# Kernel tuning notes

Hardware: AMD Instinct MI355X
Metric: run time of the kernel (lower is better)

Reference implementation:

```python
import jax, jax.numpy as jnp
import numpy as np

Q, C, T = 256, 128, 128
L = Q + C + T            # 512
D = 1024                 # d_model
H = 8                    # heads
DK = D // H              # 128 = self_attn.d_k
F = 3                    # num_latent_relations
R = 50                   # num_relation_kinds = len(relations2id)
FF = 4 * D               # feed-forward hidden
DEFAULT_QQ_ID = 0        # relations2id['q:q-default']
EPS = 1e-5


def setup_inputs():
    key = jax.random.key(0)
    ks = jax.random.split(key, 40)
    s = 0.02
    def nrm(k, shape, scale=s):
        return jax.random.normal(k, shape, jnp.float32) * scale
    inp = {
        'x': jax.random.normal(ks[0], (1, L, D), jnp.float32),
        'qc_relation': jax.random.uniform(ks[1], (Q, C, F), jnp.float32),
        'cq_relation': jax.random.uniform(ks[2], (C, Q, F), jnp.float32),
        'qt_relation': jax.random.uniform(ks[3], (Q, T, F), jnp.float32),
        'tq_relation': jax.random.uniform(ks[4], (T, Q, F), jnp.float32),
        'ct_relation': jax.random.randint(ks[5], (C + T, C + T), 0, R, jnp.int32),
        'predefined_relation': jax.random.randint(ks[6], (L, L), 0, R, jnp.int32),
        'mask': jnp.ones((1, L, L), jnp.int32),
        # relation embedding tables
        'rel_k_emb': nrm(ks[7], (R, DK)), 'rel_v_emb': nrm(ks[8], (R, DK)),
        'lqc_k': nrm(ks[9], (F, DK)), 'lqc_v': nrm(ks[10], (F, DK)),
        'lcq_k': nrm(ks[11], (F, DK)), 'lcq_v': nrm(ks[12], (F, DK)),
        'lqt_k': nrm(ks[13], (F, DK)), 'lqt_v': nrm(ks[14], (F, DK)),
        'ltq_k': nrm(ks[15], (F, DK)), 'ltq_v': nrm(ks[16], (F, DK)),
        # attention projections (torch Linear: y = x @ W.T + b)
        'Wq': nrm(ks[17], (D, D)), 'bq': jnp.zeros((D,), jnp.float32),
        'Wk': nrm(ks[18], (D, D)), 'bk': jnp.zeros((D,), jnp.float32),
        'Wv': nrm(ks[19], (D, D)), 'bv': jnp.zeros((D,), jnp.float32),
        'Wo': nrm(ks[20], (D, D)), 'bo': jnp.zeros((D,), jnp.float32),
        # layer norms
        'ln1_g': jnp.ones((D,), jnp.float32), 'ln1_b': jnp.zeros((D,), jnp.float32),
        'ln2_g': jnp.ones((D,), jnp.float32), 'ln2_b': jnp.zeros((D,), jnp.float32),
        # FFN
        'W1': nrm(ks[21], (FF, D)), 'b1': jnp.zeros((FF,), jnp.float32),
        'W2': nrm(ks[22], (D, FF)), 'b2': jnp.zeros((D,), jnp.float32),
    }
    return inp


def layer_norm(x, g, b):
    m = jnp.mean(x, -1, keepdims=True)
    v = jnp.mean((x - m) ** 2, -1, keepdims=True)
    return (x - m) * jax.lax.rsqrt(v + EPS) * g + b


def build_latent_relation(ct, qc, cq, qt, tq, emb, lqc, lcq, lqt, ltq):
    # qq block: every entry is the default-qq embedding row
    qq = jnp.broadcast_to(emb[DEFAULT_QQ_ID], (Q, Q, DK))
    qc_e = jnp.einsum('qcf,fd->qcd', qc, lqc)
    cq_e = jnp.einsum('cqf,fd->cqd', cq, lcq)
    qt_e = jnp.einsum('qtf,fd->qtd', qt, lqt)
    tq_e = jnp.einsum('tqf,fd->tqd', tq, ltq)
    ct_e = emb[ct]                                      # [(c+t),(c+t),DK]
    top = jnp.concatenate([qq, qc_e, qt_e], axis=1)      # [Q, L, DK]
    bot = jnp.concatenate([jnp.concatenate([cq_e, tq_e], 0), ct_e], axis=1)  # [C+T, L, DK]
    return jnp.concatenate([top, bot], axis=0)           # [L, L, DK]


def relation_attention(x, rel_k, rel_v, mask, Wq, bq, Wk, bk, Wv, bv, Wo, bo):
    B = x.shape[0]
    def proj(W, b):
        return (x @ W.T + b).reshape(B, L, H, DK).transpose(0, 2, 1, 3)  # [B,H,L,DK]
    q, k, v = proj(Wq, bq), proj(Wk, bk), proj(Wv, bv)
    scores = (jnp.einsum('bhid,bhjd->bhij', q, k)
              + jnp.einsum('bhid,ijd->bhij', q, rel_k)) / jnp.sqrt(jnp.float32(DK))
    scores = jnp.where(mask[:, None] == 0, jnp.float32(-1e9), scores)
    p = jax.nn.softmax(scores, axis=-1)
    o = (jnp.einsum('bhij,bhjd->bhid', p, v)
         + jnp.einsum('bhij,ijd->bhid', p, rel_v))
    o = o.transpose(0, 2, 1, 3).reshape(B, L, D)
    return o @ Wo.T + bo


def reference(x, qc_relation, cq_relation, qt_relation, tq_relation,
              ct_relation, predefined_relation, mask,
              rel_k_emb, rel_v_emb, lqc_k, lqc_v, lcq_k, lcq_v,
              lqt_k, lqt_v, ltq_k, ltq_v,
              Wq, bq, Wk, bk, Wv, bv, Wo, bo,
              ln1_g, ln1_b, ln2_g, ln2_b, W1, b1, W2, b2):
    # latent relation build + combine with predefined lookup
    rel_k = (rel_k_emb[predefined_relation]
             + build_latent_relation(ct_relation, qc_relation, cq_relation,
                                     qt_relation, tq_relation,
                                     rel_k_emb, lqc_k, lcq_k, lqt_k, ltq_k))
    rel_v = (rel_v_emb[predefined_relation]
             + build_latent_relation(ct_relation, qc_relation, cq_relation,
                                     qt_relation, tq_relation,
                                     rel_v_emb, lqc_v, lcq_v, lqt_v, ltq_v))
    # sublayer 0: pre-norm relation-biased self attention (dropout=0)
    h = x + relation_attention(layer_norm(x, ln1_g, ln1_b), rel_k, rel_v, mask,
                               Wq, bq, Wk, bk, Wv, bv, Wo, bo)
    # sublayer 1: pre-norm FFN
    y = layer_norm(h, ln2_g, ln2_b)
    ffn = jax.nn.relu(y @ W1.T + b1) @ W2.T + b2
    return h + ffn
```

## Files before the change

### kernel.cpp

```cpp
#include <hip/hip_runtime.h>
#include <hip/hip_bf16.h>

#define LL 512
#define DD 1024
#define HH 8
#define DKK 128
#define QQ 256
#define CCC 128
#define TTT 128
#define RR 50
#define FFF 4096

typedef __attribute__((ext_vector_type(8))) short short8;
typedef __attribute__((ext_vector_type(4))) float float4v;

__device__ __forceinline__ unsigned short f2bu(float f) {
  __hip_bfloat16 h = __float2bfloat16(f);
  unsigned short u; __builtin_memcpy(&u, &h, 2); return u;
}
__device__ __forceinline__ float b2f(unsigned short u) {
  unsigned int v = ((unsigned int)u) << 16;
  float f; __builtin_memcpy(&f, &v, 4); return f;
}
__device__ __forceinline__ int4 cvt8(float4 x, float4 y) {
  int4 o;
  o.x = (int)f2bu(x.x) | ((int)f2bu(x.y) << 16);
  o.y = (int)f2bu(x.z) | ((int)f2bu(x.w) << 16);
  o.z = (int)f2bu(y.x) | ((int)f2bu(y.y) << 16);
  o.w = (int)f2bu(y.z) | ((int)f2bu(y.w) << 16);
  return o;
}

__device__ __forceinline__ void lds_barrier() {
  __builtin_amdgcn_sched_barrier(0);
  __builtin_amdgcn_s_waitcnt(0xC07F);
  __builtin_amdgcn_s_barrier();
  __builtin_amdgcn_sched_barrier(0);
}

#define LOADSET(A0,A1,B0,B1,F0,F1,F2,F3,itv) { int k0v = (itv) << 6;          \
  A0 = *(const int4*)(Az + (size_t)(bm + r)*lda + k0v + gc*8);                \
  A1 = *(const int4*)(Az + (size_t)(bm + 32 + r)*lda + k0v + gc*8);           \
  if constexpr (!CONVB) {                                                     \
    B0 = *(const int4*)(Bz16 + (size_t)(bnb + r)*ldb + k0v + gc*8);           \
    if constexpr (NB > 1)                                                     \
      B1 = *(const int4*)(Bz16 + (size_t)(bnb + 32 + r)*ldb + k0v + gc*8);    \
  } else {                                                                    \
    F0 = *(const float4*)(Bz32 + (size_t)(bnb + r)*ldb + k0v + gc*8);         \
    F1 = *(const float4*)(Bz32 + (size_t)(bnb + r)*ldb + k0v + gc*8 + 4);     \
    if constexpr (NB > 1) {                                                   \
      F2 = *(const float4*)(Bz32 + (size_t)(bnb + 32 + r)*ldb + k0v + gc*8);  \
      F3 = *(const float4*)(Bz32 + (size_t)(bnb + 32 + r)*ldb + k0v + gc*8 + 4); } } }

#define STORESET2(basep,A0,A1,B0,B1,F0,F1,F2,F3) {                            \
  char* bse = (basep);                                                        \
  *(int4*)(bse + r*128 + sl*16) = A0;                                         \
  *(int4*)(bse + (32 + r)*128 + sl*16) = A1;                                  \
  if constexpr (!CONVB) {                                                     \
    *(int4*)(bse + ABYTES + r*128 + sl*16) = B0;                              \
    if constexpr (NB > 1)                                                     \
      *(int4*)(bse + ABYTES + (32 + r)*128 + sl*16) = B1;                     \
  } else {                                                                    \
    *(int4*)(bse + ABYTES + r*128 + sl*16) = cvt8(F0, F1);                    \
    if constexpr (NB > 1)                                                     \
      *(int4*)(bse + ABYTES + (32 + r)*128 + sl*16) = cvt8(F2, F3); } }

__global__ __launch_bounds__(256) void ln_bf16_kernel(const float* __restrict__ x,
    const float* __restrict__ g, const float* __restrict__ b,
    unsigned short* __restrict__ y)
{
  int row = blockIdx.x, t = threadIdx.x;
  const float4 xv = ((const float4*)(x + row*DD))[t];
  float s  = xv.x+xv.y+xv.z+xv.w;
  float ss = xv.x*xv.x+xv.y*xv.y+xv.z*xv.z+xv.w*xv.w;
  __shared__ float rs[256], rss[256];
  rs[t]=s; rss[t]=ss; __syncthreads();
  for (int st=128; st>0; st>>=1){ if (t<st){ rs[t]+=rs[t+st]; rss[t]+=rss[t+st]; } __syncthreads(); }
  float mean = rs[0] * (1.0f/DD);
  float var  = rss[0]*(1.0f/DD) - mean*mean;
  float inv  = rsqrtf(var + 1e-5f);
  float4 gv = ((const float4*)g)[t], bv = ((const float4*)b)[t];
  ushort4 ov;
  ov.x = f2bu((xv.x-mean)*inv*gv.x + bv.x);
  ov.y = f2bu((xv.y-mean)*inv*gv.y + bv.y);
  ov.z = f2bu((xv.z-mean)*inv*gv.z + bv.z);
  ov.w = f2bu((xv.w-mean)*inv*gv.w + bv.w);
  ((ushort4*)(y + row*DD))[t] = ov;
}

__global__ __launch_bounds__(256) void addbias_kernel(float* __restrict__ out,
                                                      const float* __restrict__ b2)
{
  int g = blockIdx.x*256 + threadIdx.x;
  out[g] += b2[g & (DD-1)];
}

template<int BN, int CONVB, int ZK, int OUT_BF16, int RELU, int HAS_SRC, int HAS_BIAS>
__global__ __launch_bounds__(256) void gemm_pl(
    const unsigned short* __restrict__ A, int lda, size_t sAz,
    const void* __restrict__ Bv, int ldb, size_t sBz,
    const float* __restrict__ bias,
    const float* __restrict__ src, int ldsrc, size_t sSz,
    void* __restrict__ Cv, int ldc, size_t sCz,
    int K)
{
  constexpr int BM = 64;
  constexpr int WM = 32, WN = BN/2, FM = 2, FN = WN/16;
  constexpr int NB = BN/32;
  constexpr int ABYTES = BM*128, TILE = ABYTES + BN*128;
  __shared__ char lds[2*TILE];
  int t = threadIdx.x, w = t >> 6, l = t & 63;
  size_t z = blockIdx.z;
  const unsigned short* Az = A + z*sAz;
  const unsigned short* Bz16 = (const unsigned short*)Bv + (CONVB ? 0 : z*sBz);
  const float*          Bz32 = (const float*)Bv + (CONVB ? z*sBz : 0);
  int bm = blockIdx.y*BM, bn = blockIdx.x*BN;
  int bnb = bn;
  int wm = (w>>1)*WM, wn = (w&1)*WN;

  float4v acc[FM][FN];
  #pragma unroll
  for (int m=0;m<FM;++m)
    #pragma unroll
    for (int n=0;n<FN;++n) acc[m][n] = (float4v){0.f,0.f,0.f,0.f};

  int r = t >> 3, sl = t & 7;
  int gc = sl ^ (r & 7);
  int quad = l >> 4, lrow = l & 15;
  const int nit = K >> 6;

  int4 pa0, pa1, pb0, pb1;  float4 pf0, pf1, pf2, pf3;
  int4 qa0, qa1, qb0, qb1;  float4 qf0, qf1, qf2, qf3;

  auto compute = [&](const char* base) {
    const char* ab = base;
    const char* bb = base + ABYTES;
    #pragma unroll
    for (int step=0; step<2; ++step) {
      int c = step*4 + quad;
      short8 af[FM], bf[FN];
      #pragma unroll
      for (int m=0;m<FM;++m) {
        int Rw = wm + m*16 + lrow;
        af[m] = *(const short8*)(ab + Rw*128 + ((c ^ (Rw & 7))*16));
      }
      #pragma unroll
      for (int n=0;n<FN;++n) {
        int Rw = wn + n*16 + lrow;
        bf[n] = *(const short8*)(bb + Rw*128 + ((c ^ (Rw & 7))*16));
      }
      #pragma unroll
      for (int m=0;m<FM;++m)
        #pragma unroll
        for (int n=0;n<FN;++n)
          acc[m][n] = __builtin_amdgcn_mfma_f32_16x16x32_bf16(af[m], bf[n], acc[m][n], 0, 0, 0);
    }
  };

  LOADSET(pa0,pa1,pb0,pb1,pf0,pf1,pf2,pf3, 0);
  LOADSET(qa0,qa1,qb0,qb1,qf0,qf1,qf2,qf3, 1);
  for (int it = 0; it < nit; it += 2) {
    STORESET2(lds, pa0,pa1,pb0,pb1,pf0,pf1,pf2,pf3);
    if (it + 2 < nit) LOADSET(pa0,pa1,pb0,pb1,pf0,pf1,pf2,pf3, it+2);
    lds_barrier();
    compute(lds);
    STORESET2(lds + TILE, qa0,qa1,qb0,qb1,qf0,qf1,qf2,qf3);
    if (it + 3 < nit) LOADSET(qa0,qa1,qb0,qb1,qf0,qf1,qf2,qf3, it+3);
    lds_barrier();
    compute(lds + TILE);
  }

  #pragma unroll
  for (int m=0;m<FM;++m)
    #pragma unroll
    for (int n=0;n<FN;++n)
      #pragma unroll
      for (int rg=0;rg<4;++rg) {
        int row = bm + wm + m*16 + quad*4 + rg;
        int col = bn + wn + n*16 + lrow;
        float vv = acc[m][n][rg];
        if (ZK) {
          atomicAdd(&((float*)Cv)[(size_t)row*ldc + col], vv);
        } else {
          if (HAS_BIAS) vv += bias[col];
          if (HAS_SRC)  vv += src[z*sSz + (size_t)row*ldsrc + col];
          if (RELU) vv = fmaxf(vv, 0.f);
          if (OUT_BF16) ((unsigned short*)Cv)[z*sCz + (size_t)row*ldc + col] = f2bu(vv);
          else          ((float*)Cv)[z*sCz + (size_t)row*ldc + col] = vv;
        }
      }
}

__global__ __launch_bounds__(256) void gemm_qkv_pl(
    const unsigned short* __restrict__ A,
    const float* __restrict__ Wq, const float* __restrict__ Wk,
    const float* __restrict__ Wv,
    const float* __restrict__ bq, const float* __restrict__ bk,
    const float* __restrict__ bv,
    unsigned short* __restrict__ Qh, unsigned short* __restrict__ Kh,
    unsigned short* __restrict__ Vt)
{
  constexpr int BN = 64, CONVB = 1;
  constexpr int WM = 32, WN = 32, FM = 2, FN = 2;
  constexpr int NB = 2;
  constexpr int ABYTES = 64*128, TILE = ABYTES + BN*128;
  __shared__ char lds[2*TILE];
  int t = threadIdx.x, w = t >> 6, l = t & 63;
  int bm = blockIdx.y*64, bn = blockIdx.x*BN;
  int wm = (w>>1)*WM, wn = (w&1)*WN;
  const int lda = DD, ldb = DD, nit = DD >> 6;
  const unsigned short* Az = A;
  int part0 = bn >> 10;
  const float* Bz32 = (part0==0 ? Wq : part0==1 ? Wk : Wv) + (size_t)(bn & 1023)*DD;
  const unsigned short* Bz16 = nullptr; (void)Bz16;
  int bnb = 0;

  float4v acc[FM][FN];
  #pragma unroll
  for (int m=0;m<FM;++m)
    #pragma unroll
    for (int n=0;n<FN;++n) acc[m][n] = (float4v){0.f,0.f,0.f,0.f};

  int r = t >> 3, sl = t & 7;
  int gc = sl ^ (r & 7);
  int quad = l >> 4, lrow = l & 15;

  int4 pa0, pa1, pb0, pb1;  float4 pf0, pf1, pf2, pf3;
  int4 qa0, qa1, qb0, qb1;  float4 qf0, qf1, qf2, qf3;

  auto compute = [&](const char* base) {
    const char* ab = base;
    const char* bb = base + ABYTES;
    #pragma unroll
    for (int step=0; step<2; ++step) {
      int c = step*4 + quad;
      short8 af[FM], bf[FN];
      #pragma unroll
      for (int m=0;m<FM;++m) {
        int Rw = wm + m*16 + lrow;
        af[m] = *(const short8*)(ab + Rw*128 + ((c ^ (Rw & 7))*16));
      }
      #pragma unroll
      for (int n=0;n<FN;++n) {
        int Rw = wn + n*16 + lrow;
        bf[n] = *(const short8*)(bb + Rw*128 + ((c ^ (Rw & 7))*16));
      }
      #pragma unroll
      for (int m=0;m<FM;++m)
        #pragma unroll
        for (int n=0;n<FN;++n)
          acc[m][n] = __builtin_amdgcn_mfma_f32_16x16x32_bf16(af[m], bf[n], acc[m][n], 0, 0, 0);
    }
  };

  LOADSET(pa0,pa1,pb0,pb1,pf0,pf1,pf2,pf3, 0);
  LOADSET(qa0,qa1,qb0,qb1,qf0,qf1,qf2,qf3, 1);
  for (int it = 0; it < nit; it += 2) {
    STORESET2(lds, pa0,pa1,pb0,pb1,pf0,pf1,pf2,pf3);
    if (it + 2 < nit) LOADSET(pa0,pa1,pb0,pb1,pf0,pf1,pf2,pf3, it+2);
    lds_barrier();
    compute(lds);
    STORESET2(lds + TILE, qa0,qa1,qb0,qb1,qf0,qf1,qf2,qf3);
    if (it + 3 < nit) LOADSET(qa0,qa1,qb0,qb1,qf0,qf1,qf2,qf3, it+3);
    lds_barrier();
    compute(lds + TILE);
  }

  #pragma unroll
  for (int m=0;m<FM;++m)
    #pragma unroll
    for (int n=0;n<FN;++n)
      #pragma unroll
      for (int rg=0;rg<4;++rg) {
        int row = bm + wm + m*16 + quad*4 + rg;
        int col = bn + wn + n*16 + lrow;
        int part = col >> 10, hh = (col >> 7) & 7, d = col & 127;
        const float* bp = (part==0) ? bq : (part==1) ? bk : bv;
        float vv = acc[m][n][rg] + bp[col & 1023];
        unsigned short o = f2bu(vv);
        if (part == 0)      Qh[((size_t)hh*LL + row)*DKK + d] = o;
        else if (part == 1) Kh[((size_t)hh*LL + row)*DKK + d] = o;
        else                Vt[((size_t)hh*DKK + d)*LL + row] = o;
      }
}

__global__ __launch_bounds__(64) void qtab_kernel(const unsigned short* __restrict__ Qh,
    const float* __restrict__ embk,
    const float* __restrict__ lqc, const float* __restrict__ lqt,
    const float* __restrict__ lcq, const float* __restrict__ ltq,
    float* __restrict__ qe, float* __restrict__ ql)
{
  int i = blockIdx.x, h = blockIdx.y, t = threadIdx.x;
  __shared__ float qrow[128];
  const unsigned short* qp = Qh + ((size_t)h*LL + i)*DKK;
  qrow[t] = b2f(qp[t]); qrow[t+64] = b2f(qp[t+64]);
  __syncthreads();
  if (t < RR) {
    float s = 0.f;
    #pragma unroll 8
    for (int d=0; d<128; ++d) s += qrow[d]*embk[t*128+d];
    qe[(i*HH+h)*RR + t] = s;
  } else if (t < RR + 12) {
    int u = t - RR;
    int tb = u/3, f = u - tb*3;
    const float* tab = (tb==0) ? lqc : (tb==1) ? lqt : (tb==2) ? lcq : ltq;
    const float* tr = tab + f*128;
    float s = 0.f;
    #pragma unroll 8
    for (int d=0; d<128; ++d) s += qrow[d]*tr[d];
    ql[((tb*LL + i)*HH + h)*3 + f] = s;
  }
}

__global__ __launch_bounds__(512) void softmax_kernel(
    float* __restrict__ S,
    const float* __restrict__ qe, const float* __restrict__ ql,
    const float* __restrict__ qcr, const float* __restrict__ cqr,
    const float* __restrict__ qtr, const float* __restrict__ tqr,
    const int* __restrict__ ct,   const int* __restrict__ pred,
    const int* __restrict__ mask)
{
  int i = blockIdx.x, h = blockIdx.y, j = threadIdx.x;
  __shared__ float qerow[52];
  __shared__ float red[512];
  if (j < RR) qerow[j] = qe[(i*HH+h)*RR + j];
  __syncthreads();

  float lq1[3] = {0,0,0}, lq2[3] = {0,0,0};
  if (i < QQ) {
    #pragma unroll
    for (int f=0; f<3; ++f) {
      lq1[f] = ql[((0*LL + i)*HH + h)*3 + f];
      lq2[f] = ql[((1*LL + i)*HH + h)*3 + f];
    }
  } else if (i < QQ+CCC) {
    #pragma unroll
    for (int f=0; f<3; ++f) lq1[f] = ql[((2*LL + i)*HH + h)*3 + f];
  } else {
    #pragma unroll
    for (int f=0; f<3; ++f) lq1[f] = ql[((3*LL + i)*HH + h)*3 + f];
  }

  float s = S[((size_t)h*LL + i)*LL + j];
  s += qerow[pred[i*LL + j]];
  if (i < QQ) {
    if (j < QQ) s += qerow[0];
    else if (j < QQ+CCC) { const float* r = qcr + (i*CCC + (j-QQ))*3;
      s += r[0]*lq1[0]+r[1]*lq1[1]+r[2]*lq1[2]; }
    else { const float* r = qtr + (i*TTT + (j-QQ-CCC))*3;
      s += r[0]*lq2[0]+r[1]*lq2[1]+r[2]*lq2[2]; }
  } else {
    if (j < QQ) {
      const float* r = (i < QQ+CCC) ? cqr + ((i-QQ)*QQ + j)*3
                                    : tqr + ((i-QQ-CCC)*QQ + j)*3;
      s += r[0]*lq1[0]+r[1]*lq1[1]+r[2]*lq1[2];
    } else {
      s += qerow[ct[(i-QQ)*(CCC+TTT) + (j-QQ)]];
    }
  }
  s *= 0.08838834764831845f;
  if (mask[i*LL + j] == 0) s = -1e9f;

  red[j] = s; __syncthreads();
  for (int st=256; st>0; st>>=1){ if (j<st) red[j]=fmaxf(red[j],red[j+st]); __syncthreads(); }
  float mx = red[0]; __syncthreads();
  float e = __expf(s - mx);
  red[j] = e; __syncthreads();
  for (int st=256; st>0; st>>=1){ if (j<st) red[j]+=red[j+st]; __syncthreads(); }
  float inv = 1.0f/red[0];
  ((unsigned short*)S)[((size_t)h*LL + i)*1024 + j] = f2bu(e*inv);
}

__global__ __launch_bounds__(256) void pw_kernel(
    const unsigned short* __restrict__ P,
    const float* __restrict__ embv,
    const float* __restrict__ lqc_v, const float* __restrict__ lcq_v,
    const float* __restrict__ lqt_v, const float* __restrict__ ltq_v,
    const float* __restrict__ qcr,  const float* __restrict__ cqr,
    const float* __restrict__ qtr,  const float* __restrict__ tqr,
    const int* __restrict__ ct,    const int* __restrict__ pred,
    float* __restrict__ o2)
{
  int i = blockIdx.x, t = threadIdx.x;
  __shared__ float pw8[8][56];
  __shared__ float pf1s[24], pf2s[24];
  __shared__ int predrow[512];
  __shared__ int ctrow[256];
  for (int k=t; k<8*56; k+=256) ((float*)pw8)[k] = 0.f;
  if (t < 24) { pf1s[t]=0.f; pf2s[t]=0.f; }
  for (int k=t; k<512; k+=256) predrow[k] = pred[i*LL + k];
  if (i >= QQ) { if (t < 256) ctrow[t] = ct[(i-QQ)*(CCC+TTT) + t]; }
  __syncthreads();

  int h = t >> 5, lane = t & 31;
  float qq = 0.f, l1[3] = {0,0,0}, l2[3] = {0,0,0};
  const unsigned short* Prow = P + ((size_t)h*LL + i)*1024;
  for (int jj = 0; jj < 16; ++jj) {
    int j = lane + jj*32;
    float p = b2f(Prow[j]);
    atomicAdd(&pw8[h][predrow[j]], p);
    if (i < QQ) {
      if (j < QQ) qq += p;
      else if (j < QQ+CCC) { const float* r = qcr + (i*CCC + (j-QQ))*3;
        l1[0]+=p*r[0]; l1[1]+=p*r[1]; l1[2]+=p*r[2]; }
      else { const float* r = qtr + (i*TTT + (j-QQ-CCC))*3;
        l2[0]+=p*r[0]; l2[1]+=p*r[1]; l2[2]+=p*r[2]; }
    } else {
      if (j < QQ) {
        const float* r = (i < QQ+CCC) ? cqr + ((i-QQ)*QQ + j)*3
                                      : tqr + ((i-QQ-CCC)*QQ + j)*3;
        l1[0]+=p*r[0]; l1[1]+=p*r[1]; l1[2]+=p*r[2];
      } else {
        atomicAdd(&pw8[h][ctrow[j-QQ]], p);
      }
    }
  }
  if (i < QQ) atomicAdd(&pw8[h][0], qq);
  atomicAdd(&pf1s[h*3+0], l1[0]); atomicAdd(&pf1s[h*3+1], l1[1]); atomicAdd(&pf1s[h*3+2], l1[2]);
  atomicAdd(&pf2s[h*3+0], l2[0]); atomicAdd(&pf2s[h*3+1], l2[1]); atomicAdd(&pf2s[h*3+2], l2[2]);
  __syncthreads();

  const float* tab1; const float* tab2 = nullptr;
  if (i < QQ)          { tab1 = lqc_v; tab2 = lqt_v; }
  else if (i < QQ+CCC) { tab1 = lcq_v; }
  else                 { tab1 = ltq_v; }

  for (int o = t; o < 1024; o += 256) {
    int h2 = o >> 7, d = o & 127;
    float acc = 0.f;
    #pragma unroll 5
    for (int r = 0; r < RR; ++r) acc += pw8[h2][r]*embv[r*128 + d];
    acc += pf1s[h2*3+0]*tab1[d] + pf1s[h2*3+1]*tab1[128+d] + pf1s[h2*3+2]*tab1[256+d];
    if (tab2) acc += pf2s[h2*3+0]*tab2[d] + pf2s[h2*3+1]*tab2[128+d] + pf2s[h2*3+2]*tab2[256+d];
    o2[((size_t)h2*LL + i)*DKK + d] = acc;
  }
}

extern "C" void kernel_launch(void* const* d_in, const int* in_sizes, int n_in,
                              void* d_out, int out_size, void* d_ws, size_t ws_size,
                              hipStream_t stream)
{
  const float* x    = (const float*)d_in[0];
  const float* qcr  = (const float*)d_in[1];
  const float* cqr  = (const float*)d_in[2];
  const float* qtr  = (const float*)d_in[3];
  const float* tqr  = (const float*)d_in[4];
  const int*   ct   = (const int*)d_in[5];
  const int*   pred = (const int*)d_in[6];
  const int*   mask = (const int*)d_in[7];
  const float* embk = (const float*)d_in[8];
  const float* embv = (const float*)d_in[9];
  const float* lqc_k = (const float*)d_in[10];
  const float* lqc_v = (const float*)d_in[11];
  const float* lcq_k = (const float*)d_in[12];
  const float* lcq_v = (const float*)d_in[13];
  const float* lqt_k = (const float*)d_in[14];
  const float* lqt_v = (const float*)d_in[15];
  const float* ltq_k = (const float*)d_in[16];
  const float* ltq_v = (const float*)d_in[17];
  const float* Wq = (const float*)d_in[18]; const float* bq = (const float*)d_in[19];
  const float* Wk = (const float*)d_in[20]; const float* bk = (const float*)d_in[21];
  const float* Wv = (const float*)d_in[22]; const float* bv = (const float*)d_in[23];
  const float* Wo = (const float*)d_in[24]; const float* bo = (const float*)d_in[25];
  const float* ln1_g = (const float*)d_in[26]; const float* ln1_b = (const float*)d_in[27];
  const float* ln2_g = (const float*)d_in[28]; const float* ln2_b = (const float*)d_in[29];
  const float* W1 = (const float*)d_in[30]; const float* b1 = (const float*)d_in[31];
  const float* W2 = (const float*)d_in[32]; const float* b2 = (const float*)d_in[33];
  float* out = (float*)d_out;

  float* wsf = (float*)d_ws;
  float* S    = wsf;
  float* o2   = S + (size_t)HH*LL*LL;
  float* qe   = o2 + (size_t)HH*LL*DKK;
  float* ql   = qe + LL*HH*RR;
  unsigned short* ub = (unsigned short*)(ql + 4*LL*HH*3);
  unsigned short* ybuf_b = ub;
  unsigned short* obuf_b = ybuf_b + LL*DD;
  unsigned short* Qh     = obuf_b + LL*DD;
  unsigned short* Kh     = Qh + LL*DD;
  unsigned short* Vt     = Kh + LL*DD;
  unsigned short* PS     = (unsigned short*)S;
  unsigned short* hidden = (unsigned short*)S;

  ln_bf16_kernel<<<LL, 256, 0, stream>>>(x, ln1_g, ln1_b, ybuf_b);
  gemm_qkv_pl<<<dim3(48, 8), 256, 0, stream>>>(ybuf_b, Wq, Wk, Wv, bq, bk, bv,
                                               Qh, Kh, Vt);
  qtab_kernel<<<dim3(LL, HH), 64, 0, stream>>>(Qh, embk, lqc_k, lqt_k, lcq_k, ltq_k, qe, ql);
  gemm_pl<64,0,0,0,0,0,0><<<dim3(8, 8, 8), 256, 0, stream>>>(
      Qh, DKK, (size_t)LL*DKK, Kh, DKK, (size_t)LL*DKK,
      nullptr, nullptr, 0, 0, S, LL, (size_t)LL*LL, DKK);
  softmax_kernel<<<dim3(LL, HH), 512, 0, stream>>>(S, qe, ql, qcr, cqr, qtr, tqr,
                                                   ct, pred, mask);
  pw_kernel<<<LL, 256, 0, stream>>>(PS, embv, lqc_v, lcq_v, lqt_v, ltq_v,
                                    qcr, cqr, qtr, tqr, ct, pred, o2);
  gemm_pl<32,0,0,1,0,1,0><<<dim3(4, 8, 8), 256, 0, stream>>>(
      PS, 1024, (size_t)LL*1024, Vt, LL, (size_t)DKK*LL,
      nullptr, o2, DKK, (size_t)LL*DKK, obuf_b, DD, (size_t)DKK, LL);
  gemm_pl<32,1,0,0,0,1,1><<<dim3(32, 8, 1), 256, 0, stream>>>(
      obuf_b, DD, 0, Wo, DD, 0, bo, x, DD, 0, out, DD, 0, DD);
  ln_bf16_kernel<<<LL, 256, 0, stream>>>(out, ln2_g, ln2_b, ybuf_b);
  gemm_pl<64,1,0,1,1,0,1><<<dim3(64, 8, 1), 256, 0, stream>>>(
      ybuf_b, DD, 0, W1, DD, 0, b1, nullptr, 0, 0, hidden, FFF, 0, DD);
  addbias_kernel<<<(LL*DD)/256, 256, 0, stream>>>(out, b2);
  gemm_pl<64,1,1,0,0,0,0><<<dim3(16, 8, 4), 256, 0, stream>>>(
      hidden, FFF, (size_t)1024, W2, FFF, (size_t)1024,
      nullptr, nullptr, 0, 0, out, DD, 0, 1024);
}
```

Measured before the change: 273.8 us.

## Fuse relation-value weighting into softmax and fold b2 bias into second layernorm

Merges the separate pw kernel into the softmax kernel, so each (row, head) block computes the relation-value weighted sums from the probabilities it already holds in registers. This avoids re-reading the bf16 probability matrix and saves a launch. The softmax reductions switch from an LDS tree with many barriers to wavefront shuffles. The standalone b2 bias-add kernel is folded into the second layernorm, which writes x+b2 back after reading x. The cost is LDS atomics on a small 50-entry array per block, which could contend, and the value-side work now runs per head across more blocks.

After: 276.7 us. No clear change (+1.1%).

```diff
diff --git a/kernel.cpp b/kernel.cpp
--- a/kernel.cpp
+++ b/kernel.cpp
@@ -88,11 +88,30 @@
   ((ushort4*)(y + row*DD))[t] = ov;
 }
 
-__global__ __launch_bounds__(256) void addbias_kernel(float* __restrict__ out,
-                                                      const float* __restrict__ b2)
-{
-  int g = blockIdx.x*256 + threadIdx.x;
-  out[g] += b2[g & (DD-1)];
+__global__ __launch_bounds__(256) void ln_bf16_addb_kernel(float* __restrict__ x,
+    const float* __restrict__ g, const float* __restrict__ b,
+    const float* __restrict__ b2, unsigned short* __restrict__ y)
+{
+  int row = blockIdx.x, t = threadIdx.x;
+  const float4 xv = ((const float4*)(x + row*DD))[t];
+  float s  = xv.x+xv.y+xv.z+xv.w;
+  float ss = xv.x*xv.x+xv.y*xv.y+xv.z*xv.z+xv.w*xv.w;
+  __shared__ float rs[256], rss[256];
+  rs[t]=s; rss[t]=ss; __syncthreads();
+  for (int st=128; st>0; st>>=1){ if (t<st){ rs[t]+=rs[t+st]; rss[t]+=rss[t+st]; } __syncthreads(); }
+  float mean = rs[0] * (1.0f/DD);
+  float var  = rss[0]*(1.0f/DD) - mean*mean;
+  float inv  = rsqrtf(var + 1e-5f);
+  float4 gv = ((const float4*)g)[t], bv = ((const float4*)b)[t];
+  ushort4 ov;
+  ov.x = f2bu((xv.x-mean)*inv*gv.x + bv.x);
+  ov.y = f2bu((xv.y-mean)*inv*gv.y + bv.y);
+  ov.z = f2bu((xv.z-mean)*inv*gv.z + bv.z);
+  ov.w = f2bu((xv.w-mean)*inv*gv.w + bv.w);
+  ((ushort4*)(y + row*DD))[t] = ov;
+  float4 b2v = ((const float4*)b2)[t];
+  float4 nx; nx.x = xv.x+b2v.x; nx.y = xv.y+b2v.y; nx.z = xv.z+b2v.z; nx.w = xv.w+b2v.w;
+  ((float4*)(x + row*DD))[t] = nx;
 }
 
 template<int BN, int CONVB, int ZK, int OUT_BF16, int RELU, int HAS_SRC, int HAS_BIAS>
@@ -312,19 +331,28 @@
   }
 }
 
-__global__ __launch_bounds__(512) void softmax_kernel(
+__global__ __launch_bounds__(512) void softmax_pw_kernel(
     float* __restrict__ S,
     const float* __restrict__ qe, const float* __restrict__ ql,
     const float* __restrict__ qcr, const float* __restrict__ cqr,
     const float* __restrict__ qtr, const float* __restrict__ tqr,
     const int* __restrict__ ct,   const int* __restrict__ pred,
-    const int* __restrict__ mask)
+    const int* __restrict__ mask,
+    const float* __restrict__ embv,
+    const float* __restrict__ lqc_v, const float* __restrict__ lcq_v,
+    const float* __restrict__ lqt_v, const float* __restrict__ ltq_v,
+    float* __restrict__ o2)
 {
   int i = blockIdx.x, h = blockIdx.y, j = threadIdx.x;
+  int w = j >> 6;
   __shared__ float qerow[52];
-  __shared__ float red[512];
+  __shared__ float pws[52];
+  __shared__ float pf1s[3], pf2s[3];
+  __shared__ float redw[8], redw2[8];
   if (j < RR) qerow[j] = qe[(i*HH+h)*RR + j];
-  __syncthreads();
+  if (j >= 64 && j < 64+52) pws[j-64] = 0.f;
+  if (j >= 192 && j < 195) pf1s[j-192] = 0.f;
+  if (j >= 256 && j < 259) pf2s[j-256] = 0.f;
 
   float lq1[3] = {0,0,0}, lq2[3] = {0,0,0};
   if (i < QQ) {
@@ -341,98 +369,80 @@
     for (int f=0; f<3; ++f) lq1[f] = ql[((3*LL + i)*HH + h)*3 + f];
   }
 
+  float c0=0.f, c1=0.f, c2=0.f; int route; int scat2 = 0;
+  if (i < QQ) {
+    if (j < QQ) { route = 0; scat2 = 0; }
+    else if (j < QQ+CCC) { const float* rr = qcr + (i*CCC + (j-QQ))*3;
+      c0=rr[0]; c1=rr[1]; c2=rr[2]; route = 1; }
+    else { const float* rr = qtr + (i*TTT + (j-QQ-CCC))*3;
+      c0=rr[0]; c1=rr[1]; c2=rr[2]; route = 2; }
+  } else {
+    if (j < QQ) { const float* rr = (i < QQ+CCC) ? cqr + ((i-QQ)*QQ + j)*3
+                                                 : tqr + ((i-QQ-CCC)*QQ + j)*3;
+      c0=rr[0]; c1=rr[1]; c2=rr[2]; route = 1; }
+    else { route = 0; scat2 = ct[(i-QQ)*(CCC+TTT) + (j-QQ)]; }
+  }
+  int predv = pred[i*LL + j];
   float s = S[((size_t)h*LL + i)*LL + j];
-  s += qerow[pred[i*LL + j]];
-  if (i < QQ) {
-    if (j < QQ) s += qerow[0];
-    else if (j < QQ+CCC) { const float* r = qcr + (i*CCC + (j-QQ))*3;
-      s += r[0]*lq1[0]+r[1]*lq1[1]+r[2]*lq1[2]; }
-    else { const float* r = qtr + (i*TTT + (j-QQ-CCC))*3;
-      s += r[0]*lq2[0]+r[1]*lq2[1]+r[2]*lq2[2]; }
-  } else {
-    if (j < QQ) {
-      const float* r = (i < QQ+CCC) ? cqr + ((i-QQ)*QQ + j)*3
-                                    : tqr + ((i-QQ-CCC)*QQ + j)*3;
-      s += r[0]*lq1[0]+r[1]*lq1[1]+r[2]*lq1[2];
-    } else {
-      s += qerow[ct[(i-QQ)*(CCC+TTT) + (j-QQ)]];
-    }
-  }
+  __syncthreads();
+
+  s += qerow[predv];
+  if (route == 0)      s += qerow[scat2];
+  else if (route == 1) s += c0*lq1[0] + c1*lq1[1] + c2*lq1[2];
+  else                 s += c0*lq2[0] + c1*lq2[1] + c2*lq2[2];
   s *= 0.08838834764831845f;
   if (mask[i*LL + j] == 0) s = -1e9f;
 
-  red[j] = s; __syncthreads();
-  for (int st=256; st>0; st>>=1){ if (j<st) red[j]=fmaxf(red[j],red[j+st]); __syncthreads(); }
-  float mx = red[0]; __syncthreads();
+  float m = s;
+  #pragma unroll
+  for (int off=32; off>=1; off>>=1) m = fmaxf(m, __shfl_xor(m, off));
+  if ((j & 63) == 0) redw[w] = m;
+  __syncthreads();
+  float mx = redw[0];
+  #pragma unroll
+  for (int k=1; k<8; ++k) mx = fmaxf(mx, redw[k]);
+
   float e = __expf(s - mx);
-  red[j] = e; __syncthreads();
-  for (int st=256; st>0; st>>=1){ if (j<st) red[j]+=red[j+st]; __syncthreads(); }
-  float inv = 1.0f/red[0];
-  ((unsigned short*)S)[((size_t)h*LL + i)*1024 + j] = f2bu(e*inv);
-}
-
-__global__ __launch_bounds__(256) void pw_kernel(
-    const unsigned short* __restrict__ P,
-    const float* __restrict__ embv,
-    const float* __restrict__ lqc_v, const float* __restrict__ lcq_v,
-    const float* __restrict__ lqt_v, const float* __restrict__ ltq_v,
-    const float* __restrict__ qcr,  const float* __restrict__ cqr,
-    const float* __restrict__ qtr,  const float* __restrict__ tqr,
-    const int* __restrict__ ct,    const int* __restrict__ pred,
-    float* __restrict__ o2)
-{
-  int i = blockIdx.x, t = threadIdx.x;
-  __shared__ float pw8[8][56];
-  __shared__ float pf1s[24], pf2s[24];
-  __shared__ int predrow[512];
-  __shared__ int ctrow[256];
-  for (int k=t; k<8*56; k+=256) ((float*)pw8)[k] = 0.f;
-  if (t < 24) { pf1s[t]=0.f; pf2s[t]=0.f; }
-  for (int k=t; k<512; k+=256) predrow[k] = pred[i*LL + k];
-  if (i >= QQ) { if (t < 256) ctrow[t] = ct[(i-QQ)*(CCC+TTT) + t]; }
+  float sm = e;
+  #pragma unroll
+  for (int off=32; off>=1; off>>=1) sm += __shfl_xor(sm, off);
+  if ((j & 63) == 0) redw2[w] = sm;
   __syncthreads();
-
-  int h = t >> 5, lane = t & 31;
-  float qq = 0.f, l1[3] = {0,0,0}, l2[3] = {0,0,0};
-  const unsigned short* Prow = P + ((size_t)h*LL + i)*1024;
-  for (int jj = 0; jj < 16; ++jj) {
-    int j = lane + jj*32;
-    float p = b2f(Prow[j]);
-    atomicAdd(&pw8[h][predrow[j]], p);
-    if (i < QQ) {
-      if (j < QQ) qq += p;
-      else if (j < QQ+CCC) { const float* r = qcr + (i*CCC + (j-QQ))*3;
-        l1[0]+=p*r[0]; l1[1]+=p*r[1]; l1[2]+=p*r[2]; }
-      else { const float* r = qtr + (i*TTT + (j-QQ-CCC))*3;
-        l2[0]+=p*r[0]; l2[1]+=p*r[1]; l2[2]+=p*r[2]; }
-    } else {
-      if (j < QQ) {
-        const float* r = (i < QQ+CCC) ? cqr + ((i-QQ)*QQ + j)*3
-                                      : tqr + ((i-QQ-CCC)*QQ + j)*3;
-        l1[0]+=p*r[0]; l1[1]+=p*r[1]; l1[2]+=p*r[2];
-      } else {
-        atomicAdd(&pw8[h][ctrow[j-QQ]], p);
-      }
-    }
-  }
-  if (i < QQ) atomicAdd(&pw8[h][0], qq);
-  atomicAdd(&pf1s[h*3+0], l1[0]); atomicAdd(&pf1s[h*3+1], l1[1]); atomicAdd(&pf1s[h*3+2], l1[2]);
-  atomicAdd(&pf2s[h*3+0], l2[0]); atomicAdd(&pf2s[h*3+1], l2[1]); atomicAdd(&pf2s[h*3+2], l2[2]);
+  float tot = 0.f;
+  #pragma unroll
+  for (int k=0; k<8; ++k) tot += redw2[k];
+  float p = e * (1.0f/tot);
+
+  ((unsigned short*)S)[((size_t)h*LL + i)*1024 + j] = f2bu(p);
+
+  atomicAdd(&pws[predv], p);
+  if (route == 0) atomicAdd(&pws[scat2], p);
+  float f10=0.f,f11=0.f,f12=0.f,f20=0.f,f21=0.f,f22=0.f;
+  if (route == 1) { f10=p*c0; f11=p*c1; f12=p*c2; }
+  else if (route == 2) { f20=p*c0; f21=p*c1; f22=p*c2; }
+  #pragma unroll
+  for (int off=32; off>=1; off>>=1) {
+    f10 += __shfl_xor(f10, off); f11 += __shfl_xor(f11, off); f12 += __shfl_xor(f12, off);
+    f20 += __shfl_xor(f20, off); f21 += __shfl_xor(f21, off); f22 += __shfl_xor(f22, off);
+  }
+  if ((j & 63) == 0) {
+    atomicAdd(&pf1s[0], f10); atomicAdd(&pf1s[1], f11); atomicAdd(&pf1s[2], f12);
+    atomicAdd(&pf2s[0], f20); atomicAdd(&pf2s[1], f21); atomicAdd(&pf2s[2], f22);
+  }
   __syncthreads();
 
-  const float* tab1; const float* tab2 = nullptr;
-  if (i < QQ)          { tab1 = lqc_v; tab2 = lqt_v; }
-  else if (i < QQ+CCC) { tab1 = lcq_v; }
-  else                 { tab1 = ltq_v; }
-
-  for (int o = t; o < 1024; o += 256) {
-    int h2 = o >> 7, d = o & 127;
+  if (j < 128) {
+    const float* tab1; const float* tab2 = nullptr;
+    if (i < QQ)          { tab1 = lqc_v; tab2 = lqt_v; }
+    else if (i < QQ+CCC) { tab1 = lcq_v; }
+    else                 { tab1 = ltq_v; }
+    int d = j;
     float acc = 0.f;
     #pragma unroll 5
-    for (int r = 0; r < RR; ++r) acc += pw8[h2][r]*embv[r*128 + d];
-    acc += pf1s[h2*3+0]*tab1[d] + pf1s[h2*3+1]*tab1[128+d] + pf1s[h2*3+2]*tab1[256+d];
-    if (tab2) acc += pf2s[h2*3+0]*tab2[d] + pf2s[h2*3+1]*tab2[128+d] + pf2s[h2*3+2]*tab2[256+d];
-    o2[((size_t)h2*LL + i)*DKK + d] = acc;
+    for (int r = 0; r < RR; ++r) acc += pws[r]*embv[r*128 + d];
+    acc += pf1s[0]*tab1[d] + pf1s[1]*tab1[128+d] + pf1s[2]*tab1[256+d];
+    if (tab2) acc += pf2s[0]*tab2[d] + pf2s[1]*tab2[128+d] + pf2s[2]*tab2[256+d];
+    o2[((size_t)h*LL + i)*DKK + d] = acc;
   }
 }
 
@@ -489,19 +499,17 @@
   gemm_pl<64,0,0,0,0,0,0><<<dim3(8, 8, 8), 256, 0, stream>>>(
       Qh, DKK, (size_t)LL*DKK, Kh, DKK, (size_t)LL*DKK,
       nullptr, nullptr, 0, 0, S, LL, (size_t)LL*LL, DKK);
-  softmax_kernel<<<dim3(LL, HH), 512, 0, stream>>>(S, qe, ql, qcr, cqr, qtr, tqr,
-                                                   ct, pred, mask);
-  pw_kernel<<<LL, 256, 0, stream>>>(PS, embv, lqc_v, lcq_v, lqt_v, ltq_v,
-                                    qcr, cqr, qtr, tqr, ct, pred, o2);
+  softmax_pw_kernel<<<dim3(LL, HH), 512, 0, stream>>>(
+      S, qe, ql, qcr, cqr, qtr, tqr, ct, pred, mask,
+      embv, lqc_v, lcq_v, lqt_v, ltq_v, o2);
   gemm_pl<32,0,0,1,0,1,0><<<dim3(4, 8, 8), 256, 0, stream>>>(
       PS, 1024, (size_t)LL*1024, Vt, LL, (size_t)DKK*LL,
       nullptr, o2, DKK, (size_t)LL*DKK, obuf_b, DD, (size_t)DKK, LL);
   gemm_pl<32,1,0,0,0,1,1><<<dim3(32, 8, 1), 256, 0, stream>>>(
       obuf_b, DD, 0, Wo, DD, 0, bo, x, DD, 0, out, DD, 0, DD);
-  ln_bf16_kernel<<<LL, 256, 0, stream>>>(out, ln2_g, ln2_b, ybuf_b);
+  ln_bf16_addb_kernel<<<LL, 256, 0, stream>>>(out, ln2_g, ln2_b, b2, ybuf_b);
   gemm_pl<64,1,0,1,1,0,1><<<dim3(64, 8, 1), 256, 0, stream>>>(
       ybuf_b, DD, 0, W1, DD, 0, b1, nullptr, 0, 0, hidden, FFF, 0, DD);
-  addbias_kernel<<<(LL*DD)/256, 256, 0, stream>>>(out, b2);
   gemm_pl<64,1,1,0,0,0,0><<<dim3(16, 8, 4), 256, 0, stream>>>(
       hidden, FFF, (size_t)1024, W2, FFF, (size_t)1024,
       nullptr, nullptr, 0, 0, out, DD, 0, 1024);
```
